# Kernel tuning notes

Measured on AMD Instinct MI355X. Metric: run time of the kernel, lower is better.

## Reference

```python
import jax, jax.numpy as jnp
import numpy as np

NUM_STATES = 32768
NUM_LABELS = 64
BATCH = 512


def setup_inputs() -> dict:
    key = jax.random.key(0)
    k1, k2, k3, k4 = jax.random.split(key, 4)
    f = jax.random.normal(k1, (BATCH, NUM_LABELS), dtype=jnp.float32)
    # legal_state: binary indicator matrix [num_states, num_labels]
    S = jax.random.randint(k2, (NUM_STATES, NUM_LABELS), 0, 2).astype(jnp.float32)
    y = jax.random.uniform(k3, (BATCH, NUM_LABELS), dtype=jnp.float32)
    mask = jax.random.randint(k4, (BATCH, NUM_LABELS), 0, 2).astype(jnp.float32)
    return {"f": f, "S": S, "y": y, "mask": mask}


def reference(f, S, y, mask):
    # potential[s, b] = sum_i S[s, i] * f[b, i]
    potential = jnp.einsum('si,bi->sb', S, f)
    # stable softmax over the state axis (replaces exp/max/sum in original)
    P = jax.nn.softmax(potential, axis=0)  # [num_states, batch]
    # pMargin[b, i] = sum_{s: S[s,i]>0} P[s, b]  ->  indicator-matrix GEMM
    pMargin = jnp.einsum('sb,si->bi', P, S)  # [batch, num_labels]
    # per-column BCE (torch BCELoss clamps log at -100), masked, mean over batch
    logp = jnp.clip(jnp.log(pMargin), -100.0, None)
    log1mp = jnp.clip(jnp.log(1.0 - pMargin), -100.0, None)
    bce = -(y * logp + (1.0 - y) * log1mp) * mask  # [batch, num_labels]
    loss = jnp.sum(jnp.mean(bce, axis=0))  # sum over columns of per-column means
    return loss, pMargin
```

## Files before the change

kernel.cpp:

```cpp
#include <hip/hip_runtime.h>
#include <hip/hip_bf16.h>
#include <math.h>

#define N_STATES 32768
#define N_LABELS 64
#define N_BATCH  512

#define ZP_F     1024
#define UP_F     65536
#define SB_BYTE  8650752u
#define STB_BYTE 12845056u

typedef __attribute__((ext_vector_type(8))) short          bfrag;
typedef __attribute__((ext_vector_type(4))) short          bhalf;
typedef __attribute__((ext_vector_type(4))) float          f32x4;
typedef __attribute__((ext_vector_type(8))) unsigned short u16x8;

static __device__ __forceinline__ unsigned short f2bf(float x) {
    __hip_bfloat16 h = __float2bfloat16(x);
    return *reinterpret_cast<unsigned short*>(&h);
}
static __device__ __forceinline__ float bf2f(unsigned short u) {
    __hip_bfloat16 h;
    *reinterpret_cast<unsigned short*>(&h) = u;
    return __bfloat162float(h);
}

typedef __attribute__((address_space(1))) const unsigned char g_u8;
typedef __attribute__((address_space(3))) unsigned char       l_u8;
static __device__ __forceinline__ void dma16(const void* g, void* l) {
    __builtin_amdgcn_global_load_lds((g_u8*)g, (l_u8*)l, 16, 0, 0);
}

__global__ __launch_bounds__(256) void prep_kernel(
    const float* __restrict__ S, float* __restrict__ ws) {
    const int tb = blockIdx.x;
    const int t  = threadIdx.x;

    __shared__ alignas(16) unsigned short Sl[64 * 72];

    unsigned short* SbW = (unsigned short*)((char*)ws + SB_BYTE);
    unsigned short* StW = (unsigned short*)((char*)ws + STB_BYTE);

    const int r = t >> 2;
    const int q = t & 3;
    const int m = r & 7;

    const float4* p4 = reinterpret_cast<const float4*>(
        S + ((size_t)(tb * 64 + r)) * N_LABELS + q * 16);
    float4 v0 = p4[0], v1 = p4[1], v2 = p4[2], v3 = p4[3];
    float vf[16] = {v0.x,v0.y,v0.z,v0.w, v1.x,v1.y,v1.z,v1.w,
                    v2.x,v2.y,v2.z,v2.w, v3.x,v3.y,v3.z,v3.w};
    u16x8 lo8, hi8;
    #pragma unroll
    for (int j = 0; j < 8; j++) { lo8[j] = f2bf(vf[j]); hi8[j] = f2bf(vf[8 + j]); }

    *(u16x8*)&Sl[r * 72 + q * 16]     = lo8;
    *(u16x8*)&Sl[r * 72 + q * 16 + 8] = hi8;

    {
        unsigned short* dst = SbW + (size_t)tb * 4096 + r * 64 + (((2 * q) ^ (m & 6)) * 8);
        if (m & 1) { *(u16x8*)dst = hi8; *(u16x8*)(dst + 8) = lo8; }
        else       { *(u16x8*)dst = lo8; *(u16x8*)(dst + 8) = hi8; }
    }
    __syncthreads();

    const int i  = r;
    const int mi = i & 7;
    u16x8 tlo, thi;
    #pragma unroll
    for (int j = 0; j < 8; j++) {
        tlo[j] = Sl[(16 * q + j)     * 72 + i];
        thi[j] = Sl[(16 * q + 8 + j) * 72 + i];
    }
    {
        unsigned short* dst = StW + (size_t)tb * 4096 + i * 64 + (((2 * q) ^ (mi & 6)) * 8);
        if (mi & 1) { *(u16x8*)dst = thi; *(u16x8*)(dst + 8) = tlo; }
        else        { *(u16x8*)dst = tlo; *(u16x8*)(dst + 8) = thi; }
    }
}

__global__ __launch_bounds__(256, 2) void fused_kernel(
    const float* __restrict__ f, float* __restrict__ ws,
    float* __restrict__ out) {
    __shared__ alignas(16) unsigned char smem[66560];

    const char* SbG = (const char*)ws + SB_BYTE;
    const char* StG = (const char*)ws + STB_BYTE;

    const int t     = threadIdx.x;
    const int lane  = t & 63;
    const int w     = t >> 6;
    const int x     = lane & 15;
    const int quad  = lane >> 4;
    const int mm    = x & 7;
    const int btile = blockIdx.x >> 6;
    const int chunk = blockIdx.x & 63;
    const int tile0 = chunk * 8;

    bfrag fh[4][2], fl[4][2];
    float Mv[4];
    #pragma unroll
    for (int nt = 0; nt < 4; nt++) {
        const float4* fp = reinterpret_cast<const float4*>(
            f + ((size_t)(btile * 64 + nt * 16 + x)) * N_LABELS);
        float msum = 0.f;
        #pragma unroll
        for (int kh = 0; kh < 2; kh++) {
            float4 a = fp[kh * 8 + quad * 2];
            float4 b = fp[kh * 8 + quad * 2 + 1];
            float vv[8] = {a.x,a.y,a.z,a.w, b.x,b.y,b.z,b.w};
            #pragma unroll
            for (int j = 0; j < 8; j++) {
                msum += fmaxf(vv[j], 0.f);
                unsigned short h = f2bf(vv[j]);
                fh[nt][kh][j] = (short)h;
                fl[nt][kh][j] = (short)f2bf(vv[j] - bf2f(h));
            }
        }
        msum += __shfl_xor(msum, 16, 64);
        msum += __shfl_xor(msum, 32, 64);
        Mv[nt] = msum;
    }

    f32x4 Uacc[16];
    #pragma unroll
    for (int e = 0; e < 16; e++) Uacc[e] = (f32x4){0.f, 0.f, 0.f, 0.f};
    float zacc[4] = {0.f, 0.f, 0.f, 0.f};

    auto stage = [&](int tile, int buf) {
        size_t gb = (size_t)tile * 8192 + (size_t)w * 2048 + (size_t)lane * 16;
        int lo = w * 2048;
        dma16(SbG + gb,        smem + buf * 8192 + lo);
        dma16(SbG + gb + 1024, smem + buf * 8192 + lo + 1024);
        dma16(StG + gb,        smem + 16384 + buf * 8192 + lo);
        dma16(StG + gb + 1024, smem + 16384 + buf * 8192 + lo + 1024);
    };

    stage(tile0 + 0, 0);
    stage(tile0 + 1, 1);
    asm volatile("s_waitcnt vmcnt(4)" ::: "memory");
    asm volatile("s_barrier" ::: "memory");

    #pragma unroll
    for (int st = 0; st < 8; st++) {
        const int cur = st & 1;
        const unsigned short* Sb = (const unsigned short*)(smem + cur * 8192);
        const unsigned short* St = (const unsigned short*)(smem + 16384 + cur * 8192);

        bfrag a0 = *(const bfrag*)(Sb + (16 * w + x) * 64 + ((quad ^ mm) * 8));
        bfrag a1 = *(const bfrag*)(Sb + (16 * w + x) * 64 + (((quad + 4) ^ mm) * 8));

        bfrag A8[4];
        #pragma unroll
        for (int it = 0; it < 4; it++) {
            bhalf a4 = *(const bhalf*)(St + (16 * it + x) * 64 +
                         (((2 * w + (quad >> 1)) ^ mm) * 8) + 4 * (quad & 1));
            bfrag tmp = {a4[0], a4[1], a4[2], a4[3], 0, 0, 0, 0};
            A8[it] = tmp;
        }

        #pragma unroll
        for (int nt = 0; nt < 4; nt++) {
            f32x4 acc = (f32x4){0.f, 0.f, 0.f, 0.f};
            acc = __builtin_amdgcn_mfma_f32_16x16x32_bf16(a0, fh[nt][0], acc, 0, 0, 0);
            acc = __builtin_amdgcn_mfma_f32_16x16x32_bf16(a1, fh[nt][1], acc, 0, 0, 0);
            acc = __builtin_amdgcn_mfma_f32_16x16x32_bf16(a0, fl[nt][0], acc, 0, 0, 0);
            acc = __builtin_amdgcn_mfma_f32_16x16x32_bf16(a1, fl[nt][1], acc, 0, 0, 0);
            float e0 = __expf(acc[0] - Mv[nt]);
            float e1 = __expf(acc[1] - Mv[nt]);
            float e2 = __expf(acc[2] - Mv[nt]);
            float e3 = __expf(acc[3] - Mv[nt]);
            zacc[nt] += (e0 + e1) + (e2 + e3);
            bfrag Bf = {(short)f2bf(e0), (short)f2bf(e1),
                        (short)f2bf(e2), (short)f2bf(e3), 0, 0, 0, 0};
            #pragma unroll
            for (int it = 0; it < 4; it++)
                Uacc[it * 4 + nt] =
                    __builtin_amdgcn_mfma_f32_16x16x32_bf16(A8[it], Bf, Uacc[it * 4 + nt], 0, 0, 0);
        }

        if (st < 6) {
            asm volatile("s_barrier" ::: "memory");
            stage(tile0 + st + 2, cur);
            asm volatile("s_waitcnt vmcnt(4)" ::: "memory");
            asm volatile("s_barrier" ::: "memory");
        } else if (st == 6) {
            asm volatile("s_waitcnt vmcnt(0)" ::: "memory");
            asm volatile("s_barrier" ::: "memory");
        }
    }

    __syncthreads();
    float* mg  = (float*)smem;
    float* zsh = (float*)(smem + 65536);
    #pragma unroll
    for (int e = 0; e < 16; e++) {
        #pragma unroll
        for (int r = 0; r < 4; r++)
            mg[w * 4096 + (e * 4 + r) * 64 + lane] = Uacc[e][r];
    }
    #pragma unroll
    for (int nt = 0; nt < 4; nt++) {
        float v = zacc[nt];
        v += __shfl_down(v, 32, 64);
        v += __shfl_down(v, 16, 64);
        if (quad == 0) zsh[w * 64 + nt * 16 + x] = v;
    }
    __syncthreads();

    float* Up = ws + UP_F;
    #pragma unroll
    for (int k = 0; k < 16; k++) {
        int idx = k * 256 + t;
        int e  = idx >> 6;
        int ln = idx & 63;
        int it = e >> 4, nt = (e >> 2) & 3, r = e & 3;
        int i  = it * 16 + (ln >> 4) * 4 + r;
        int b  = nt * 16 + (ln & 15);
        float s = mg[idx] + mg[4096 + idx] + mg[8192 + idx] + mg[12288 + idx];
        Up[((btile * 64 + i) * 64 + chunk) * 64 + b] = s;
    }
    if (t < 64) {
        float z = zsh[t] + zsh[64 + t] + zsh[128 + t] + zsh[192 + t];
        (ws + ZP_F)[(btile * 64 + chunk) * 64 + t] = z;
    }
    if (blockIdx.x == 0 && t == 0) out[0] = 0.f;
}

__global__ __launch_bounds__(256) void finalize_kernel(
    const float* __restrict__ ws, const float* __restrict__ y,
    const float* __restrict__ mask, float* __restrict__ out) {
    const int i     = blockIdx.x >> 1;
    const int b     = ((blockIdx.x & 1) << 8) + threadIdx.x;
    const int btile = b >> 6;
    const int bl    = b & 63;

    const float* zp = ws + ZP_F + (btile * 64) * 64 + bl;
    const float* up = ws + UP_F + ((btile * 64 + i) * 64) * 64 + bl;
    float z = 0.f, u = 0.f;
    #pragma unroll 8
    for (int c = 0; c < 64; c++) { z += zp[c * 64]; u += up[c * 64]; }

    float p = fminf(fmaxf(u / z, 0.f), 1.f);
    const int idx = b * 64 + i;
    out[1 + idx] = p;

    float lp  = fmaxf(logf(p), -100.f);
    float l1p = fmaxf(logf(1.f - p), -100.f);
    float yy = y[idx];
    float bce = -(yy * lp + (1.f - yy) * l1p) * mask[idx] * (1.f / (float)N_BATCH);

    float v = bce;
    #pragma unroll
    for (int off = 32; off > 0; off >>= 1) v += __shfl_down(v, off, 64);
    __shared__ float wsum[4];
    if ((threadIdx.x & 63) == 0) wsum[threadIdx.x >> 6] = v;
    __syncthreads();
    if (threadIdx.x == 0)
        atomicAdd(&out[0], wsum[0] + wsum[1] + wsum[2] + wsum[3]);
}

extern "C" void kernel_launch(void* const* d_in, const int* in_sizes, int n_in,
                              void* d_out, int out_size, void* d_ws, size_t ws_size,
                              hipStream_t stream) {
    const float* f    = (const float*)d_in[0];
    const float* S    = (const float*)d_in[1];
    const float* y    = (const float*)d_in[2];
    const float* mask = (const float*)d_in[3];
    float* out = (float*)d_out;
    float* ws  = (float*)d_ws;

    prep_kernel<<<512, 256, 0, stream>>>(S, ws);
    fused_kernel<<<512, 256, 0, stream>>>(f, ws, out);
    finalize_kernel<<<128, 256, 0, stream>>>(ws, y, mask, out);
}
```

Measured before the change: 94.79 us.

## Drop S prep kernel; load fp32 S directly into registers in fused kernel

Removes the separate prep kernel that converted S to swizzled bf16 row and transposed copies in workspace. The fused kernel now reads fp32 S straight from global memory per tile, converting to bf16 in registers, and drops the LDS double-buffered DMA pipeline and its barriers. This saves a kernel launch and the prep pass over S, but each block now reads fp32 (twice the bytes), the transposed column loads are strided scalar accesses, and there is no longer any prefetch overlap.

```diff
diff --git a/kernel.cpp b/kernel.cpp
--- a/kernel.cpp
+++ b/kernel.cpp
@@ -8,13 +8,9 @@
 
 #define ZP_F     1024
 #define UP_F     65536
-#define SB_BYTE  8650752u
-#define STB_BYTE 12845056u
 
-typedef __attribute__((ext_vector_type(8))) short          bfrag;
-typedef __attribute__((ext_vector_type(4))) short          bhalf;
-typedef __attribute__((ext_vector_type(4))) float          f32x4;
-typedef __attribute__((ext_vector_type(8))) unsigned short u16x8;
+typedef __attribute__((ext_vector_type(8))) short bfrag;
+typedef __attribute__((ext_vector_type(4))) float f32x4;
 
 static __device__ __forceinline__ unsigned short f2bf(float x) {
     __hip_bfloat16 h = __float2bfloat16(x);
@@ -26,77 +22,18 @@
     return __bfloat162float(h);
 }
 
-typedef __attribute__((address_space(1))) const unsigned char g_u8;
-typedef __attribute__((address_space(3))) unsigned char       l_u8;
-static __device__ __forceinline__ void dma16(const void* g, void* l) {
-    __builtin_amdgcn_global_load_lds((g_u8*)g, (l_u8*)l, 16, 0, 0);
-}
-
-__global__ __launch_bounds__(256) void prep_kernel(
-    const float* __restrict__ S, float* __restrict__ ws) {
-    const int tb = blockIdx.x;
-    const int t  = threadIdx.x;
-
-    __shared__ alignas(16) unsigned short Sl[64 * 72];
-
-    unsigned short* SbW = (unsigned short*)((char*)ws + SB_BYTE);
-    unsigned short* StW = (unsigned short*)((char*)ws + STB_BYTE);
-
-    const int r = t >> 2;
-    const int q = t & 3;
-    const int m = r & 7;
-
-    const float4* p4 = reinterpret_cast<const float4*>(
-        S + ((size_t)(tb * 64 + r)) * N_LABELS + q * 16);
-    float4 v0 = p4[0], v1 = p4[1], v2 = p4[2], v3 = p4[3];
-    float vf[16] = {v0.x,v0.y,v0.z,v0.w, v1.x,v1.y,v1.z,v1.w,
-                    v2.x,v2.y,v2.z,v2.w, v3.x,v3.y,v3.z,v3.w};
-    u16x8 lo8, hi8;
-    #pragma unroll
-    for (int j = 0; j < 8; j++) { lo8[j] = f2bf(vf[j]); hi8[j] = f2bf(vf[8 + j]); }
-
-    *(u16x8*)&Sl[r * 72 + q * 16]     = lo8;
-    *(u16x8*)&Sl[r * 72 + q * 16 + 8] = hi8;
-
-    {
-        unsigned short* dst = SbW + (size_t)tb * 4096 + r * 64 + (((2 * q) ^ (m & 6)) * 8);
-        if (m & 1) { *(u16x8*)dst = hi8; *(u16x8*)(dst + 8) = lo8; }
-        else       { *(u16x8*)dst = lo8; *(u16x8*)(dst + 8) = hi8; }
-    }
-    __syncthreads();
-
-    const int i  = r;
-    const int mi = i & 7;
-    u16x8 tlo, thi;
-    #pragma unroll
-    for (int j = 0; j < 8; j++) {
-        tlo[j] = Sl[(16 * q + j)     * 72 + i];
-        thi[j] = Sl[(16 * q + 8 + j) * 72 + i];
-    }
-    {
-        unsigned short* dst = StW + (size_t)tb * 4096 + i * 64 + (((2 * q) ^ (mi & 6)) * 8);
-        if (mi & 1) { *(u16x8*)dst = thi; *(u16x8*)(dst + 8) = tlo; }
-        else        { *(u16x8*)dst = tlo; *(u16x8*)(dst + 8) = thi; }
-    }
-}
-
 __global__ __launch_bounds__(256, 2) void fused_kernel(
-    const float* __restrict__ f, float* __restrict__ ws,
-    float* __restrict__ out) {
+    const float* __restrict__ f, const float* __restrict__ S,
+    float* __restrict__ ws, float* __restrict__ out) {
     __shared__ alignas(16) unsigned char smem[66560];
-
-    const char* SbG = (const char*)ws + SB_BYTE;
-    const char* StG = (const char*)ws + STB_BYTE;
 
     const int t     = threadIdx.x;
     const int lane  = t & 63;
     const int w     = t >> 6;
     const int x     = lane & 15;
     const int quad  = lane >> 4;
-    const int mm    = x & 7;
     const int btile = blockIdx.x >> 6;
     const int chunk = blockIdx.x & 63;
-    const int tile0 = chunk * 8;
 
     bfrag fh[4][2], fl[4][2];
     float Mv[4];
@@ -128,35 +65,30 @@
     for (int e = 0; e < 16; e++) Uacc[e] = (f32x4){0.f, 0.f, 0.f, 0.f};
     float zacc[4] = {0.f, 0.f, 0.f, 0.f};
 
-    auto stage = [&](int tile, int buf) {
-        size_t gb = (size_t)tile * 8192 + (size_t)w * 2048 + (size_t)lane * 16;
-        int lo = w * 2048;
-        dma16(SbG + gb,        smem + buf * 8192 + lo);
-        dma16(SbG + gb + 1024, smem + buf * 8192 + lo + 1024);
-        dma16(StG + gb,        smem + 16384 + buf * 8192 + lo);
-        dma16(StG + gb + 1024, smem + 16384 + buf * 8192 + lo + 1024);
-    };
-
-    stage(tile0 + 0, 0);
-    stage(tile0 + 1, 1);
-    asm volatile("s_waitcnt vmcnt(4)" ::: "memory");
-    asm volatile("s_barrier" ::: "memory");
-
     #pragma unroll
     for (int st = 0; st < 8; st++) {
-        const int cur = st & 1;
-        const unsigned short* Sb = (const unsigned short*)(smem + cur * 8192);
-        const unsigned short* St = (const unsigned short*)(smem + 16384 + cur * 8192);
+        const int s0 = (chunk * 8 + st) * 64;
 
-        bfrag a0 = *(const bfrag*)(Sb + (16 * w + x) * 64 + ((quad ^ mm) * 8));
-        bfrag a1 = *(const bfrag*)(Sb + (16 * w + x) * 64 + (((quad + 4) ^ mm) * 8));
+        const float* Arow = S + (size_t)(s0 + 16 * w + x) * N_LABELS + quad * 8;
+        float4 r0 = *(const float4*)(Arow);
+        float4 r1 = *(const float4*)(Arow + 4);
+        float4 r2 = *(const float4*)(Arow + 32);
+        float4 r3 = *(const float4*)(Arow + 36);
+        bfrag a0 = {(short)f2bf(r0.x), (short)f2bf(r0.y), (short)f2bf(r0.z), (short)f2bf(r0.w),
+                    (short)f2bf(r1.x), (short)f2bf(r1.y), (short)f2bf(r1.z), (short)f2bf(r1.w)};
+        bfrag a1 = {(short)f2bf(r2.x), (short)f2bf(r2.y), (short)f2bf(r2.z), (short)f2bf(r2.w),
+                    (short)f2bf(r3.x), (short)f2bf(r3.y), (short)f2bf(r3.z), (short)f2bf(r3.w)};
 
+        const float* Acol = S + (size_t)(s0 + 16 * w + 4 * quad) * N_LABELS + x;
         bfrag A8[4];
         #pragma unroll
         for (int it = 0; it < 4; it++) {
-            bhalf a4 = *(const bhalf*)(St + (16 * it + x) * 64 +
-                         (((2 * w + (quad >> 1)) ^ mm) * 8) + 4 * (quad & 1));
-            bfrag tmp = {a4[0], a4[1], a4[2], a4[3], 0, 0, 0, 0};
+            float c0 = Acol[0 * 64 + it * 16];
+            float c1 = Acol[1 * 64 + it * 16];
+            float c2 = Acol[2 * 64 + it * 16];
+            float c3 = Acol[3 * 64 + it * 16];
+            bfrag tmp = {(short)f2bf(c0), (short)f2bf(c1),
+                         (short)f2bf(c2), (short)f2bf(c3), 0, 0, 0, 0};
             A8[it] = tmp;
         }
 
@@ -179,19 +111,8 @@
                 Uacc[it * 4 + nt] =
                     __builtin_amdgcn_mfma_f32_16x16x32_bf16(A8[it], Bf, Uacc[it * 4 + nt], 0, 0, 0);
         }
-
-        if (st < 6) {
-            asm volatile("s_barrier" ::: "memory");
-            stage(tile0 + st + 2, cur);
-            asm volatile("s_waitcnt vmcnt(4)" ::: "memory");
-            asm volatile("s_barrier" ::: "memory");
-        } else if (st == 6) {
-            asm volatile("s_waitcnt vmcnt(0)" ::: "memory");
-            asm volatile("s_barrier" ::: "memory");
-        }
     }
 
-    __syncthreads();
     float* mg  = (float*)smem;
     float* zsh = (float*)(smem + 65536);
     #pragma unroll
@@ -271,7 +192,6 @@
     float* out = (float*)d_out;
     float* ws  = (float*)d_ws;
 
-    prep_kernel<<<512, 256, 0, stream>>>(S, ws);
-    fused_kernel<<<512, 256, 0, stream>>>(f, ws, out);
+    fused_kernel<<<512, 256, 0, stream>>>(f, S, ws, out);
     finalize_kernel<<<128, 256, 0, stream>>>(ws, y, mask, out);
 }
```

Result: no change. 96.23 us (+1.5%).
